# Kernel optimization log

Measured on AMD Instinct MI355X. Metric: run time of the kernel, lower is better.

## Reference

```python
import jax, jax.numpy as jnp
import numpy as np

B, L, D = 2, 2048, 2048
H, KV, HD = 16, 4, 128          # num_heads, num_kv_heads, head_dim
RD = HD // 2                    # rope_dim = 64
G = H // KV                     # GQA groups


def _rotate_half(t):
    t1, t2 = jnp.split(t, 2, axis=-1)
    return jnp.concatenate([-t2, t1], axis=-1)


def setup_inputs() -> dict:
    key = jax.random.key(0)
    ks = jax.random.split(key, 8)
    x = jax.random.normal(ks[0], (B, L, D), dtype=jnp.float32)
    # proper RoPE cos/sin tables of width RD (half-rotation layout)
    inv_freq = 1.0 / (10000.0 ** (np.arange(0, RD, 2, dtype=np.float32) / RD))
    pos = np.arange(L, dtype=np.float32)
    freqs = np.outer(pos, inv_freq)               # [L, RD/2]
    emb = np.concatenate([freqs, freqs], axis=-1)  # [L, RD]
    cos = jnp.broadcast_to(jnp.cos(emb)[None], (B, L, RD)).astype(jnp.float32)
    sin = jnp.broadcast_to(jnp.sin(emb)[None], (B, L, RD)).astype(jnp.float32)
    s = 0.02
    Wq = jax.random.normal(ks[1], (H * HD, D), dtype=jnp.float32) * s
    bq = jnp.zeros((H * HD,), dtype=jnp.float32)
    Wkv = jax.random.normal(ks[2], (KV * HD, D), dtype=jnp.float32) * s
    bkv = jnp.zeros((KV * HD,), dtype=jnp.float32)
    Wrk = jax.random.normal(ks[3], (RD, D), dtype=jnp.float32) * s
    brk = jnp.zeros((RD,), dtype=jnp.float32)
    Wo = jax.random.normal(ks[4], (D, H * HD), dtype=jnp.float32) * s
    bo = jnp.zeros((D,), dtype=jnp.float32)
    return {"x": x, "cos": cos, "sin": sin, "Wq": Wq, "bq": bq,
            "Wkv": Wkv, "bkv": bkv, "Wrk": Wrk, "brk": brk, "Wo": Wo, "bo": bo}


def reference(x, cos, sin, Wq, bq, Wkv, bkv, Wrk, brk, Wo, bo):
    Bx, Lx, _ = x.shape
    q = (x @ Wq.T + bq).reshape(Bx, Lx, H, HD)            # [B,L,H,HD]
    kv = (x @ Wkv.T + bkv).reshape(Bx, Lx, KV, HD)        # [B,L,KV,HD]
    q_nope, q_rope = q[..., : HD - RD], q[..., HD - RD:]  # [.,HD-RD],[.,RD]
    k_rope = (x @ Wrk.T + brk).reshape(Bx, Lx, 1, RD)     # [B,L,1,RD]
    c = cos[:, :, None, :]
    s = sin[:, :, None, :]
    q_rope = q_rope * c + _rotate_half(q_rope) * s
    k_rope = k_rope * c + _rotate_half(k_rope) * s
    k_rope = jnp.broadcast_to(k_rope, (Bx, Lx, KV, RD))   # tied across kv heads
    q_states = jnp.concatenate([q_nope, q_rope], axis=-1)  # [B,L,H,HD]
    kv_tied = kv[..., : HD - RD]
    k_states = jnp.concatenate([kv_tied, k_rope], axis=-1)  # [B,L,KV,HD]
    v_states = kv                                            # cat(kv_tied, tail) == kv
    # GQA causal attention, scale 1/sqrt(HD)
    qg = q_states.reshape(Bx, Lx, KV, G, HD)
    scale = 1.0 / jnp.sqrt(jnp.asarray(HD, dtype=x.dtype))
    scores = jnp.einsum('bqkgd,bskd->bkgqs', qg, k_states) * scale
    mask = jnp.tril(jnp.ones((Lx, Lx), dtype=bool))
    scores = jnp.where(mask[None, None, None], scores, jnp.finfo(scores.dtype).min)
    probs = jax.nn.softmax(scores, axis=-1)
    out = jnp.einsum('bkgqs,bskd->bqkgd', probs, v_states)
    out = out.reshape(Bx, Lx, H * HD)
    return out @ Wo.T + bo
```

## Files before the change

kernel.cpp:

```cpp
#include <hip/hip_runtime.h>
#include <hip/hip_bf16.h>

#define BB   2
#define LL   2048
#define DD   2048
#define HH   16
#define KVH  4
#define HDD  128
#define RDD  64
#define MM   (BB*LL)

typedef __attribute__((ext_vector_type(4))) float f32x4;
typedef __attribute__((ext_vector_type(8))) short bf16x8;
typedef unsigned short u16;

static __device__ __forceinline__ u16 f2b(float f) {
  __hip_bfloat16 b = __float2bfloat16(f);
  return *(const u16*)&b;
}

static __device__ __forceinline__ void gload_lds16(const void* g, void* l) {
  __builtin_amdgcn_global_load_lds(
      (const __attribute__((address_space(1))) unsigned int*)g,
      (__attribute__((address_space(3))) unsigned int*)l, 16, 0, 0);
}

#define QSCALE 0.1275174313f

__global__ __launch_bounds__(256) void cast_all(const float* __restrict__ x,
                                                const float* __restrict__ Wq,
                                                const float* __restrict__ Wkv,
                                                const float* __restrict__ Wrk,
                                                const float* __restrict__ Wo,
                                                u16* __restrict__ xb, u16* __restrict__ Wqb,
                                                u16* __restrict__ Wkvb, u16* __restrict__ Wrkb,
                                                u16* __restrict__ Wob) {
  const int i = blockIdx.x * 256 + threadIdx.x;
  const float* src; u16* dst; int off;
  if (i < 2097152)      { src = x;   dst = xb;   off = i; }
  else if (i < 3145728) { src = Wq;  dst = Wqb;  off = i - 2097152; }
  else if (i < 3407872) { src = Wkv; dst = Wkvb; off = i - 3145728; }
  else if (i < 3440640) { src = Wrk; dst = Wrkb; off = i - 3407872; }
  else                  { src = Wo;  dst = Wob;  off = i - 3440640; }
  float4 v = ((const float4*)src)[off];
  ushort4 o;
  o.x = f2b(v.x); o.y = f2b(v.y); o.z = f2b(v.z); o.w = f2b(v.w);
  ((ushort4*)dst)[off] = o;
}

__global__ __launch_bounds__(256) void gemm128(const u16* __restrict__ A,
                                               const u16* __restrict__ W,
                                               const float* __restrict__ bias,
                                               float* __restrict__ C,
                                               int M, int N, int K) {
  __shared__ u16 As[128 * 32];
  __shared__ u16 Bs[128 * 32];
  const int w = threadIdx.x >> 6, lane = threadIdx.x & 63;
  const int r = lane & 15, hi = lane >> 4, rg = hi * 4;
  const int wm = w >> 1, wn = w & 1;
  const int m0 = blockIdx.y * 128, n0 = blockIdx.x * 128;
  const int srow = w * 32 + (lane >> 2);
  const int scb  = (lane & 3) * 16;
  f32x4 acc[4][4];
#pragma unroll
  for (int i = 0; i < 4; ++i)
#pragma unroll
    for (int j = 0; j < 4; ++j) acc[i][j] = (f32x4){0.f, 0.f, 0.f, 0.f};

  for (int k0 = 0; k0 < K; k0 += 32) {
#pragma unroll
    for (int i = 0; i < 2; ++i) {
      gload_lds16((const char*)(A + (size_t)(m0 + srow + i * 16) * K + k0) + scb,
                  (char*)As + (w * 2 + i) * 1024);
      gload_lds16((const char*)(W + (size_t)(n0 + srow + i * 16) * K + k0) + scb,
                  (char*)Bs + (w * 2 + i) * 1024);
    }
    __syncthreads();
    bf16x8 a[4], b[4];
#pragma unroll
    for (int i = 0; i < 4; ++i)
      a[i] = *(const bf16x8*)((const char*)As + (wm * 64 + i * 16 + r) * 64 + hi * 16);
#pragma unroll
    for (int j = 0; j < 4; ++j)
      b[j] = *(const bf16x8*)((const char*)Bs + (wn * 64 + j * 16 + r) * 64 + hi * 16);
#pragma unroll
    for (int i = 0; i < 4; ++i)
#pragma unroll
      for (int j = 0; j < 4; ++j)
        acc[i][j] = __builtin_amdgcn_mfma_f32_16x16x32_bf16(a[i], b[j], acc[i][j], 0, 0, 0);
    __syncthreads();
  }
#pragma unroll
  for (int j = 0; j < 4; ++j) {
    const float bv = bias[n0 + wn * 64 + j * 16 + r];
#pragma unroll
    for (int i = 0; i < 4; ++i)
#pragma unroll
      for (int ii = 0; ii < 4; ++ii)
        C[(size_t)(m0 + wm * 64 + i * 16 + rg + ii) * N + n0 + wn * 64 + j * 16 + r] =
            acc[i][j][ii] + bv;
  }
}

__global__ __launch_bounds__(256) void gemm_q_fused(const u16* __restrict__ A,
                                                    const u16* __restrict__ W,
                                                    const float* __restrict__ bias,
                                                    const float* __restrict__ cosb,
                                                    const float* __restrict__ sinb,
                                                    u16* __restrict__ Qb) {
  __shared__ u16 As[128 * 32];
  __shared__ u16 Bs[128 * 32];
  const int w = threadIdx.x >> 6, lane = threadIdx.x & 63;
  const int r = lane & 15, hi = lane >> 4, rg = hi * 4;
  const int wm = w >> 1, wn = w & 1;
  const int h = blockIdx.x;
  const int m0 = blockIdx.y * 128, n0 = h * 128;
  const int srow = w * 32 + (lane >> 2);
  const int scb  = (lane & 3) * 16;
  f32x4 acc[4][4];
#pragma unroll
  for (int i = 0; i < 4; ++i)
#pragma unroll
    for (int j = 0; j < 4; ++j) acc[i][j] = (f32x4){0.f, 0.f, 0.f, 0.f};

  for (int k0 = 0; k0 < DD; k0 += 32) {
#pragma unroll
    for (int i = 0; i < 2; ++i) {
      gload_lds16((const char*)(A + (size_t)(m0 + srow + i * 16) * DD + k0) + scb,
                  (char*)As + (w * 2 + i) * 1024);
      gload_lds16((const char*)(W + (size_t)(n0 + srow + i * 16) * DD + k0) + scb,
                  (char*)Bs + (w * 2 + i) * 1024);
    }
    __syncthreads();
    bf16x8 a[4], b[4];
#pragma unroll
    for (int i = 0; i < 4; ++i)
      a[i] = *(const bf16x8*)((const char*)As + (wm * 64 + i * 16 + r) * 64 + hi * 16);
#pragma unroll
    for (int j = 0; j < 4; ++j)
      b[j] = *(const bf16x8*)((const char*)Bs + (wn * 64 + j * 16 + r) * 64 + hi * 16);
#pragma unroll
    for (int i = 0; i < 4; ++i)
#pragma unroll
      for (int j = 0; j < 4; ++j)
        acc[i][j] = __builtin_amdgcn_mfma_f32_16x16x32_bf16(a[i], b[j], acc[i][j], 0, 0, 0);
    __syncthreads();
  }

  const int b = m0 >> 11;
  const int lbase = (m0 & 2047) + wm * 64;
  u16* Qimg = Qb + (size_t)((b * 16 + h) * 128) * 2048;
  if (wn == 0) {
#pragma unroll
    for (int j = 0; j < 4; ++j) {
      const int d = j * 16 + r;
      const float bv = bias[h * 128 + d];
#pragma unroll
      for (int i = 0; i < 4; ++i)
#pragma unroll
        for (int ii = 0; ii < 4; ++ii) {
          const int l = lbase + i * 16 + rg + ii;
          Qimg[(size_t)(l >> 4) * 2048 + (d >> 5) * 512 + ((d >> 3) & 3) * 128 +
               (l & 15) * 8 + (d & 7)] = f2b((acc[i][j][ii] + bv) * QSCALE);
        }
    }
  } else {
#pragma unroll
    for (int jp = 0; jp < 2; ++jp) {
      const int dd0 = jp * 16 + r;
      const int dd1 = dd0 + 32;
      const float bv0 = bias[h * 128 + 64 + dd0];
      const float bv1 = bias[h * 128 + 64 + dd1];
#pragma unroll
      for (int i = 0; i < 4; ++i)
#pragma unroll
        for (int ii = 0; ii < 4; ++ii) {
          const int l = lbase + i * 16 + rg + ii;
          const size_t nb = (size_t)(b * 2048 + l) * 64;
          const float c0 = cosb[nb + dd0], s0 = sinb[nb + dd0];
          const float c1 = cosb[nb + dd1], s1 = sinb[nb + dd1];
          const float a0 = acc[i][jp][ii] + bv0;
          const float a1 = acc[i][jp + 2][ii] + bv1;
          const float v0 = (a0 * c0 - a1 * s0) * QSCALE;
          const float v1 = (a1 * c1 + a0 * s1) * QSCALE;
          const int d0f = 64 + dd0, d1f = 64 + dd1;
          const size_t rowoff = (size_t)(l >> 4) * 2048 + (l & 15) * 8;
          Qimg[rowoff + (d0f >> 5) * 512 + ((d0f >> 3) & 3) * 128 + (d0f & 7)] = f2b(v0);
          Qimg[rowoff + (d1f >> 5) * 512 + ((d1f >> 3) & 3) * 128 + (d1f & 7)] = f2b(v1);
        }
    }
  }
}

__global__ __launch_bounds__(256) void gemm_kv_fused(const u16* __restrict__ A,
                                                     const u16* __restrict__ W,
                                                     const float* __restrict__ bias,
                                                     u16* __restrict__ Kb,
                                                     u16* __restrict__ VTb) {
  __shared__ u16 As[128 * 32];
  __shared__ u16 Bs[128 * 32];
  const int w = threadIdx.x >> 6, lane = threadIdx.x & 63;
  const int r = lane & 15, hi = lane >> 4, rg = hi * 4;
  const int wm = w >> 1, wn = w & 1;
  const int c = blockIdx.x;
  const int m0 = blockIdx.y * 128, n0 = c * 128;
  const int srow = w * 32 + (lane >> 2);
  const int scb  = (lane & 3) * 16;
  f32x4 acc[4][4];
#pragma unroll
  for (int i = 0; i < 4; ++i)
#pragma unroll
    for (int j = 0; j < 4; ++j) acc[i][j] = (f32x4){0.f, 0.f, 0.f, 0.f};

  for (int k0 = 0; k0 < DD; k0 += 32) {
#pragma unroll
    for (int i = 0; i < 2; ++i) {
      gload_lds16((const char*)(A + (size_t)(m0 + srow + i * 16) * DD + k0) + scb,
                  (char*)As + (w * 2 + i) * 1024);
      gload_lds16((const char*)(W + (size_t)(n0 + srow + i * 16) * DD + k0) + scb,
                  (char*)Bs + (w * 2 + i) * 1024);
    }
    __syncthreads();
    bf16x8 a[4], b[4];
#pragma unroll
    for (int i = 0; i < 4; ++i)
      a[i] = *(const bf16x8*)((const char*)As + (wm * 64 + i * 16 + r) * 64 + hi * 16);
#pragma unroll
    for (int j = 0; j < 4; ++j)
      b[j] = *(const bf16x8*)((const char*)Bs + (wn * 64 + j * 16 + r) * 64 + hi * 16);
#pragma unroll
    for (int i = 0; i < 4; ++i)
#pragma unroll
      for (int j = 0; j < 4; ++j)
        acc[i][j] = __builtin_amdgcn_mfma_f32_16x16x32_bf16(a[i], b[j], acc[i][j], 0, 0, 0);
    __syncthreads();
  }

  const int b = m0 >> 11;
  const int lbase = (m0 & 2047) + wm * 64;
  u16* Kimg = Kb + (size_t)(b * KVH + c) * 32 * 8192;
  u16* Vimg = VTb + (size_t)(b * KVH + c) * 32 * 8192;
#pragma unroll
  for (int j = 0; j < 4; ++j) {
    const int d = wn * 64 + j * 16 + r;
    const float bv = bias[c * 128 + d];
#pragma unroll
    for (int i = 0; i < 4; ++i)
#pragma unroll
      for (int ii = 0; ii < 4; ++ii) {
        const int l = lbase + i * 16 + rg + ii;
        const u16 bf = f2b(acc[i][j][ii] + bv);
        const int lt = l & 63;
        Vimg[(size_t)(l >> 6) * 8192 + ((d >> 4) * 2 + ((lt >> 5) & 1)) * 512 +
             ((lt >> 2) & 3) * 128 + (d & 15) * 8 + ((lt >> 4) & 1) * 4 + (lt & 3)] = bf;
        if (wn == 0)
          Kimg[(size_t)(l >> 6) * 8192 + ((lt >> 4) & 3) * 2048 + (d >> 5) * 512 +
               ((d >> 3) & 3) * 128 + (lt & 15) * 8 + (d & 7)] = bf;
      }
  }
}

__global__ __launch_bounds__(256) void gemm_rk_fused(const u16* __restrict__ A,
                                                     const u16* __restrict__ Wrkb,
                                                     const float* __restrict__ brk,
                                                     const float* __restrict__ cosb,
                                                     const float* __restrict__ sinb,
                                                     u16* __restrict__ Kb) {
  __shared__ f32x4 red[4][2][64];
  const int w = threadIdx.x >> 6, lane = threadIdx.x & 63;
  const int bx = blockIdx.x;
  const int m0 = blockIdx.y * 16;
  const int r = lane & 15;
  const int kq = (lane >> 4) * 8;
  const u16* ap  = A + (size_t)(m0 + r) * DD + kq;
  const u16* wp0 = Wrkb + (size_t)(bx * 16 + r) * DD + kq;
  const u16* wp1 = Wrkb + (size_t)(bx * 16 + 32 + r) * DD + kq;
  f32x4 acc0 = {0.f, 0.f, 0.f, 0.f}, acc1 = {0.f, 0.f, 0.f, 0.f};
  for (int k = w * 512; k < w * 512 + 512; k += 32) {
    bf16x8 a  = *(const bf16x8*)(ap + k);
    bf16x8 b0 = *(const bf16x8*)(wp0 + k);
    bf16x8 b1 = *(const bf16x8*)(wp1 + k);
    acc0 = __builtin_amdgcn_mfma_f32_16x16x32_bf16(a, b0, acc0, 0, 0, 0);
    acc1 = __builtin_amdgcn_mfma_f32_16x16x32_bf16(a, b1, acc1, 0, 0, 0);
  }
  red[w][0][lane] = acc0;
  red[w][1][lane] = acc1;
  __syncthreads();
  if (w == 0) {
#pragma unroll
    for (int ww = 1; ww < 4; ++ww) {
      acc0 += red[ww][0][lane];
      acc1 += red[ww][1][lane];
    }
    const int rg = (lane >> 4) * 4;
    const int dd0 = bx * 16 + r, dd1 = dd0 + 32;
    const float bv0 = brk[dd0], bv1 = brk[dd1];
    const int d0f = 64 + dd0, d1f = 64 + dd1;
#pragma unroll
    for (int i = 0; i < 4; ++i) {
      const int n = m0 + rg + i;
      const int b = n >> 11, l = n & 2047;
      const size_t nb = (size_t)n * 64;
      const float c0 = cosb[nb + dd0], s0 = sinb[nb + dd0];
      const float c1 = cosb[nb + dd1], s1 = sinb[nb + dd1];
      const float a0 = acc0[i] + bv0;
      const float a1 = acc1[i] + bv1;
      const u16 v0 = f2b(a0 * c0 - a1 * s0);
      const u16 v1 = f2b(a1 * c1 + a0 * s1);
      const int lt = l & 63;
      const size_t loff = (size_t)(l >> 6) * 8192 + ((lt >> 4) & 3) * 2048 + (lt & 15) * 8;
#pragma unroll
      for (int c = 0; c < 4; ++c) {
        u16* Kimg = Kb + (size_t)(b * KVH + c) * 32 * 8192;
        Kimg[loff + (d0f >> 5) * 512 + ((d0f >> 3) & 3) * 128 + (d0f & 7)] = v0;
        Kimg[loff + (d1f >> 5) * 512 + ((d1f >> 3) & 3) * 128 + (d1f & 7)] = v1;
      }
    }
  }
}

static __device__ __forceinline__ void stage_g(const u16* Kt, const u16* Vt,
                                               char* GB, int buf, int wg, int lane) {
#pragma unroll
  for (int i = 0; i < 4; ++i) {
    const int j = wg * 4 + i;
    gload_lds16(Kt + (size_t)j * 512 + lane * 8, (u16*)(GB + buf * 16384) + j * 512);
    gload_lds16(Vt + (size_t)j * 512 + lane * 8, (u16*)(GB + 32768 + buf * 16384) + j * 512);
  }
}

__global__ __launch_bounds__(512, 2) void attn_mfma10(const u16* __restrict__ Qb,
                                                      const u16* __restrict__ Kb,
                                                      const u16* __restrict__ VTb,
                                                      u16* __restrict__ attn_bf) {
  const int id = blockIdx.x;
  const int g = id & 31;
  const int s = id >> 5;
  const int bc = g & 7, hlow = g >> 3;
  const int b = bc >> 2, c = bc & 3;
  const int h = c * 4 + hlow;
  const int bh = b * 16 + h;
  const int w = threadIdx.x >> 6, lane = threadIdx.x & 63;
  const int r = lane & 15, hi = lane >> 4, rg = hi * 4;
  const int grp = w >> 2, wg = w & 3;

  __shared__ __align__(16) char LB[131072];
  char* GB = LB + grp * 65536;

  const u16* Ktg = Kb + (size_t)(b * KVH + c) * 32 * 8192;
  const u16* Vtg = VTb + (size_t)(b * KVH + c) * 32 * 8192;

  for (int ss = 0; ss < 2; ++ss) {
    const int qb = ss ? s : (15 - s);
    const int q0 = qb * 128 + wg * 32;
    const int half = qb + 1;
    const int tb = grp ? half : 0;

    bf16x8 qf[2][4];
#pragma unroll
    for (int qs = 0; qs < 2; ++qs) {
      const u16* qtb = Qb + (size_t)(bh * 128 + qb * 8 + wg * 2 + qs) * 2048;
#pragma unroll
      for (int ks = 0; ks < 4; ++ks)
        qf[qs][ks] = *(const bf16x8*)(qtb + ks * 512 + lane * 8);
    }

    float m_[2] = {-3.0e38f, -3.0e38f}, l_[2] = {0.f, 0.f};
    f32x4 o[2][8];
#pragma unroll
    for (int qs = 0; qs < 2; ++qs)
#pragma unroll
      for (int t = 0; t < 8; ++t) o[qs][t] = (f32x4){0.f, 0.f, 0.f, 0.f};

    stage_g(Ktg + (size_t)tb * 8192, Vtg + (size_t)tb * 8192, GB, 0, wg, lane);
    __syncthreads();
    int cur = 0;

    for (int t = 0; t < half; ++t) {
      if (t + 1 < half)
        stage_g(Ktg + (size_t)(tb + t + 1) * 8192, Vtg + (size_t)(tb + t + 1) * 8192,
                GB, cur ^ 1, wg, lane);
      const int s0 = (tb + t) * 64;

      if (s0 <= q0 + 31) {
        const u16* Kl = (const u16*)(GB + cur * 16384);
        const u16* Vl = (const u16*)(GB + 32768 + cur * 16384);

        f32x4 st[2][4];
#pragma unroll
        for (int qs = 0; qs < 2; ++qs)
#pragma unroll
          for (int tt = 0; tt < 4; ++tt) st[qs][tt] = (f32x4){0.f, 0.f, 0.f, 0.f};
        __builtin_amdgcn_s_setprio(1);
#pragma unroll
        for (int tt = 0; tt < 4; ++tt) {
          bf16x8 kf[4];
#pragma unroll
          for (int ks = 0; ks < 4; ++ks)
            kf[ks] = *(const bf16x8*)(Kl + tt * 2048 + ks * 512 + lane * 8);
#pragma unroll
          for (int qs = 0; qs < 2; ++qs)
#pragma unroll
            for (int ks = 0; ks < 4; ++ks)
              st[qs][tt] = __builtin_amdgcn_mfma_f32_16x16x32_bf16(kf[ks], qf[qs][ks], st[qs][tt], 0, 0, 0);
        }
        __builtin_amdgcn_s_setprio(0);

        if (s0 + 63 > q0) {
#pragma unroll
          for (int qs = 0; qs < 2; ++qs)
#pragma unroll
            for (int tt = 0; tt < 4; ++tt)
#pragma unroll
              for (int i = 0; i < 4; ++i)
                if (s0 + tt * 16 + rg + i > q0 + qs * 16 + r) st[qs][tt][i] = -3.0e38f;
        }

        float vmax[2];
#pragma unroll
        for (int qs = 0; qs < 2; ++qs) {
          float v = st[qs][0][0];
#pragma unroll
          for (int tt = 0; tt < 4; ++tt)
#pragma unroll
            for (int i = 0; i < 4; ++i) v = fmaxf(v, st[qs][tt][i]);
          v = fmaxf(v, __shfl_xor(v, 16));
          v = fmaxf(v, __shfl_xor(v, 32));
          vmax[qs] = v;
        }
        const float grow = fmaxf(vmax[0] - m_[0], vmax[1] - m_[1]);
        if (!__all(grow <= 11.54f)) {
#pragma unroll
          for (int qs = 0; qs < 2; ++qs) {
            const float mn = fmaxf(m_[qs], vmax[qs]);
            const float cf = exp2f(m_[qs] - mn);
            l_[qs] *= cf;
            m_[qs] = mn;
#pragma unroll
            for (int tt = 0; tt < 8; ++tt)
#pragma unroll
              for (int i = 0; i < 4; ++i) o[qs][tt][i] *= cf;
          }
        }
        bf16x8 pa[2][2];
#pragma unroll
        for (int qs = 0; qs < 2; ++qs) {
          float ps = 0.f;
#pragma unroll
          for (int tt = 0; tt < 4; ++tt)
#pragma unroll
            for (int i = 0; i < 4; ++i) {
              st[qs][tt][i] = exp2f(st[qs][tt][i] - m_[qs]);
              ps += st[qs][tt][i];
            }
          ps += __shfl_xor(ps, 16);
          ps += __shfl_xor(ps, 32);
          l_[qs] += ps;
#pragma unroll
          for (int kb = 0; kb < 2; ++kb) {
            bf16x8 v;
#pragma unroll
            for (int jj = 0; jj < 8; ++jj)
              v[jj] = (short)f2b(st[qs][2 * kb + (jj >> 2)][jj & 3]);
            pa[qs][kb] = v;
          }
        }

        __builtin_amdgcn_s_setprio(1);
#pragma unroll
        for (int tt = 0; tt < 8; ++tt) {
#pragma unroll
          for (int kb = 0; kb < 2; ++kb) {
            bf16x8 vf = *(const bf16x8*)(Vl + tt * 1024 + kb * 512 + lane * 8);
#pragma unroll
            for (int qs = 0; qs < 2; ++qs)
              o[qs][tt] = __builtin_amdgcn_mfma_f32_16x16x32_bf16(pa[qs][kb], vf, o[qs][tt], 0, 0, 0);
          }
        }
        __builtin_amdgcn_s_setprio(0);
      }

      __syncthreads();
      cur ^= 1;
    }

    float2* mlp = (float2*)(LB + 65536);
    if (hi == 0) {
      mlp[(w * 2 + 0) * 16 + r] = make_float2(m_[0], l_[0]);
      mlp[(w * 2 + 1) * 16 + r] = make_float2(m_[1], l_[1]);
    }
    __syncthreads();
    float lC[2], asc[2];
#pragma unroll
    for (int qs = 0; qs < 2; ++qs) {
      const float2 p = mlp[((w ^ 4) * 2 + qs) * 16 + r];
      const float mn = fmaxf(m_[qs], p.x);
      const float a1 = exp2f(m_[qs] - mn);
      lC[qs] = l_[qs] * a1 + p.y * exp2f(p.x - mn);
      asc[qs] = a1;
    }
#pragma unroll
    for (int qs = 0; qs < 2; ++qs) {
      float ai[4];
#pragma unroll
      for (int i = 0; i < 4; ++i) ai[i] = __shfl(asc[qs], (lane & 48) + rg + i);
#pragma unroll
      for (int tt = 0; tt < 8; ++tt)
#pragma unroll
        for (int i = 0; i < 4; ++i) o[qs][tt][i] *= ai[i];
    }
    if (grp == 1) {
#pragma unroll
      for (int qs = 0; qs < 2; ++qs)
#pragma unroll
        for (int tt = 0; tt < 8; ++tt)
          *(f32x4*)(LB + wg * 16384 + (qs * 8 + tt) * 1024 + lane * 16) = o[qs][tt];
    }
    __syncthreads();
    if (grp == 0) {
#pragma unroll
      for (int qs = 0; qs < 2; ++qs) {
#pragma unroll
        for (int tt = 0; tt < 8; ++tt)
          o[qs][tt] += *(const f32x4*)(LB + wg * 16384 + (qs * 8 + tt) * 1024 + lane * 16);
        const float il = 1.f / lC[qs];
        float inv[4];
#pragma unroll
        for (int i = 0; i < 4; ++i) inv[i] = __shfl(il, (lane & 48) + rg + i);
        u16* op = attn_bf + (size_t)(b * LL + q0 + qs * 16 + rg) * DD + h * HDD;
#pragma unroll
        for (int tt = 0; tt < 8; ++tt)
#pragma unroll
          for (int i = 0; i < 4; ++i)
            op[(size_t)i * DD + tt * 16 + r] = f2b(o[qs][tt][i] * inv[i]);
      }
    }
    __syncthreads();
  }
}

extern "C" void kernel_launch(void* const* d_in, const int* in_sizes, int n_in,
                              void* d_out, int out_size, void* d_ws, size_t ws_size,
                              hipStream_t stream) {
  const float* x    = (const float*)d_in[0];
  const float* cosb = (const float*)d_in[1];
  const float* sinb = (const float*)d_in[2];
  const float* Wq   = (const float*)d_in[3];
  const float* bq   = (const float*)d_in[4];
  const float* Wkv  = (const float*)d_in[5];
  const float* bkv  = (const float*)d_in[6];
  const float* Wrk  = (const float*)d_in[7];
  const float* brk  = (const float*)d_in[8];
  const float* Wo   = (const float*)d_in[9];
  const float* bo   = (const float*)d_in[10];
  float* out = (float*)d_out;

  char* ws = (char*)d_ws;
  u16*   Qb    = (u16*)(ws);
  u16*   attn_bf = (u16*)(ws + 16777216);
  u16*   xb    = (u16*)(ws + 33554432);
  u16*   Wqb   = (u16*)(ws + 50331648);
  u16*   Wob   = (u16*)(ws + 58720256);
  u16*   Wkvb  = (u16*)(ws + 67108864);
  u16*   Wrkb  = (u16*)(ws + 69206016);
  u16*   Kb    = (u16*)(ws + 70516736);
  u16*   VTb   = (u16*)(ws + 74711040);

  cast_all<<<17536, 256, 0, stream>>>(x, Wq, Wkv, Wrk, Wo, xb, Wqb, Wkvb, Wrkb, Wob);

  gemm_q_fused<<<dim3(HH, MM / 128), 256, 0, stream>>>(xb, Wqb, bq, cosb, sinb, Qb);
  gemm_kv_fused<<<dim3(KVH, MM / 128), 256, 0, stream>>>(xb, Wkvb, bkv, Kb, VTb);
  gemm_rk_fused<<<dim3(2, MM / 16), 256, 0, stream>>>(xb, Wrkb, brk, cosb, sinb, Kb);

  attn_mfma10<<<dim3(256), 512, 0, stream>>>(Qb, Kb, VTb, attn_bf);

  gemm128<<<dim3(DD / 128, MM / 128), 256, 0, stream>>>(attn_bf, Wob, bo, out, MM, DD, DD);
}
```

Baseline: 231.5 us.

## Split attention KV range across four wave groups with 32-row KV tiles

The attention kernel now runs 1024 threads per block, with four wave groups each covering a quarter of the causal KV range, instead of two groups covering halves. KV tiles shrink from 64 to 32 rows, so the K/V image layouts written by the projection GEMMs change to match. The final softmax merge combines four partial (m,l) pairs and reduces outputs through LDS in two stages. This is meant to shorten the per-block serial KV loop and add waves for latency hiding, at the cost of one block per CU, smaller MFMA batches per sync, and a longer merge.

Result: slower. 363.1 us (+56.9%).

```diff
diff --git a/kernel.cpp b/kernel.cpp
--- a/kernel.cpp
+++ b/kernel.cpp
@@ -238,8 +238,8 @@
 
   const int b = m0 >> 11;
   const int lbase = (m0 & 2047) + wm * 64;
-  u16* Kimg = Kb + (size_t)(b * KVH + c) * 32 * 8192;
-  u16* Vimg = VTb + (size_t)(b * KVH + c) * 32 * 8192;
+  u16* Kimg = Kb + (size_t)(b * KVH + c) * 64 * 4096;
+  u16* Vimg = VTb + (size_t)(b * KVH + c) * 64 * 4096;
 #pragma unroll
   for (int j = 0; j < 4; ++j) {
     const int d = wn * 64 + j * 16 + r;
@@ -250,11 +250,11 @@
       for (int ii = 0; ii < 4; ++ii) {
         const int l = lbase + i * 16 + rg + ii;
         const u16 bf = f2b(acc[i][j][ii] + bv);
-        const int lt = l & 63;
-        Vimg[(size_t)(l >> 6) * 8192 + ((d >> 4) * 2 + ((lt >> 5) & 1)) * 512 +
-             ((lt >> 2) & 3) * 128 + (d & 15) * 8 + ((lt >> 4) & 1) * 4 + (lt & 3)] = bf;
+        const int lt = l & 31;
+        Vimg[(size_t)(l >> 5) * 4096 + (d >> 4) * 512 + ((lt >> 2) & 3) * 128 +
+             (d & 15) * 8 + ((lt >> 4) & 1) * 4 + (lt & 3)] = bf;
         if (wn == 0)
-          Kimg[(size_t)(l >> 6) * 8192 + ((lt >> 4) & 3) * 2048 + (d >> 5) * 512 +
+          Kimg[(size_t)(l >> 5) * 4096 + ((lt >> 4) & 1) * 2048 + (d >> 5) * 512 +
                ((d >> 3) & 3) * 128 + (lt & 15) * 8 + (d & 7)] = bf;
       }
   }
@@ -307,11 +307,11 @@
       const float a1 = acc1[i] + bv1;
       const u16 v0 = f2b(a0 * c0 - a1 * s0);
       const u16 v1 = f2b(a1 * c1 + a0 * s1);
-      const int lt = l & 63;
-      const size_t loff = (size_t)(l >> 6) * 8192 + ((lt >> 4) & 3) * 2048 + (lt & 15) * 8;
+      const int lt = l & 31;
+      const size_t loff = (size_t)(l >> 5) * 4096 + ((lt >> 4) & 1) * 2048 + (lt & 15) * 8;
 #pragma unroll
       for (int c = 0; c < 4; ++c) {
-        u16* Kimg = Kb + (size_t)(b * KVH + c) * 32 * 8192;
+        u16* Kimg = Kb + (size_t)(b * KVH + c) * 64 * 4096;
         Kimg[loff + (d0f >> 5) * 512 + ((d0f >> 3) & 3) * 128 + (d0f & 7)] = v0;
         Kimg[loff + (d1f >> 5) * 512 + ((d1f >> 3) & 3) * 128 + (d1f & 7)] = v1;
       }
@@ -322,17 +322,17 @@
 static __device__ __forceinline__ void stage_g(const u16* Kt, const u16* Vt,
                                                char* GB, int buf, int wg, int lane) {
 #pragma unroll
-  for (int i = 0; i < 4; ++i) {
-    const int j = wg * 4 + i;
-    gload_lds16(Kt + (size_t)j * 512 + lane * 8, (u16*)(GB + buf * 16384) + j * 512);
-    gload_lds16(Vt + (size_t)j * 512 + lane * 8, (u16*)(GB + 32768 + buf * 16384) + j * 512);
-  }
-}
-
-__global__ __launch_bounds__(512, 2) void attn_mfma10(const u16* __restrict__ Qb,
-                                                      const u16* __restrict__ Kb,
-                                                      const u16* __restrict__ VTb,
-                                                      u16* __restrict__ attn_bf) {
+  for (int i = 0; i < 2; ++i) {
+    const int j = wg * 2 + i;
+    gload_lds16(Kt + (size_t)j * 512 + lane * 8, (u16*)(GB + buf * 8192) + j * 512);
+    gload_lds16(Vt + (size_t)j * 512 + lane * 8, (u16*)(GB + 16384 + buf * 8192) + j * 512);
+  }
+}
+
+__global__ __launch_bounds__(1024, 1) void attn_mfma12(const u16* __restrict__ Qb,
+                                                       const u16* __restrict__ Kb,
+                                                       const u16* __restrict__ VTb,
+                                                       u16* __restrict__ attn_bf) {
   const int id = blockIdx.x;
   const int g = id & 31;
   const int s = id >> 5;
@@ -344,17 +344,17 @@
   const int r = lane & 15, hi = lane >> 4, rg = hi * 4;
   const int grp = w >> 2, wg = w & 3;
 
-  __shared__ __align__(16) char LB[131072];
-  char* GB = LB + grp * 65536;
-
-  const u16* Ktg = Kb + (size_t)(b * KVH + c) * 32 * 8192;
-  const u16* Vtg = VTb + (size_t)(b * KVH + c) * 32 * 8192;
+  __shared__ __align__(16) char LB[135168];
+  char* GB = LB + grp * 32768;
+
+  const u16* Ktg = Kb + (size_t)(b * KVH + c) * 64 * 4096;
+  const u16* Vtg = VTb + (size_t)(b * KVH + c) * 64 * 4096;
 
   for (int ss = 0; ss < 2; ++ss) {
     const int qb = ss ? s : (15 - s);
     const int q0 = qb * 128 + wg * 32;
     const int half = qb + 1;
-    const int tb = grp ? half : 0;
+    const int tb = grp * half;
 
     bf16x8 qf[2][4];
 #pragma unroll
@@ -372,28 +372,28 @@
 #pragma unroll
       for (int t = 0; t < 8; ++t) o[qs][t] = (f32x4){0.f, 0.f, 0.f, 0.f};
 
-    stage_g(Ktg + (size_t)tb * 8192, Vtg + (size_t)tb * 8192, GB, 0, wg, lane);
+    stage_g(Ktg + (size_t)tb * 4096, Vtg + (size_t)tb * 4096, GB, 0, wg, lane);
     __syncthreads();
     int cur = 0;
 
     for (int t = 0; t < half; ++t) {
       if (t + 1 < half)
-        stage_g(Ktg + (size_t)(tb + t + 1) * 8192, Vtg + (size_t)(tb + t + 1) * 8192,
+        stage_g(Ktg + (size_t)(tb + t + 1) * 4096, Vtg + (size_t)(tb + t + 1) * 4096,
                 GB, cur ^ 1, wg, lane);
-      const int s0 = (tb + t) * 64;
+      const int s0 = (tb + t) * 32;
 
       if (s0 <= q0 + 31) {
-        const u16* Kl = (const u16*)(GB + cur * 16384);
-        const u16* Vl = (const u16*)(GB + 32768 + cur * 16384);
-
-        f32x4 st[2][4];
+        const u16* Kl = (const u16*)(GB + cur * 8192);
+        const u16* Vl = (const u16*)(GB + 16384 + cur * 8192);
+
+        f32x4 st[2][2];
 #pragma unroll
         for (int qs = 0; qs < 2; ++qs)
 #pragma unroll
-          for (int tt = 0; tt < 4; ++tt) st[qs][tt] = (f32x4){0.f, 0.f, 0.f, 0.f};
+          for (int tt = 0; tt < 2; ++tt) st[qs][tt] = (f32x4){0.f, 0.f, 0.f, 0.f};
         __builtin_amdgcn_s_setprio(1);
 #pragma unroll
-        for (int tt = 0; tt < 4; ++tt) {
+        for (int tt = 0; tt < 2; ++tt) {
           bf16x8 kf[4];
 #pragma unroll
           for (int ks = 0; ks < 4; ++ks)
@@ -406,11 +406,11 @@
         }
         __builtin_amdgcn_s_setprio(0);
 
-        if (s0 + 63 > q0) {
+        if (s0 + 31 > q0) {
 #pragma unroll
           for (int qs = 0; qs < 2; ++qs)
 #pragma unroll
-            for (int tt = 0; tt < 4; ++tt)
+            for (int tt = 0; tt < 2; ++tt)
 #pragma unroll
               for (int i = 0; i < 4; ++i)
                 if (s0 + tt * 16 + rg + i > q0 + qs * 16 + r) st[qs][tt][i] = -3.0e38f;
@@ -421,7 +421,7 @@
         for (int qs = 0; qs < 2; ++qs) {
           float v = st[qs][0][0];
 #pragma unroll
-          for (int tt = 0; tt < 4; ++tt)
+          for (int tt = 0; tt < 2; ++tt)
 #pragma unroll
             for (int i = 0; i < 4; ++i) v = fmaxf(v, st[qs][tt][i]);
           v = fmaxf(v, __shfl_xor(v, 16));
@@ -442,12 +442,12 @@
               for (int i = 0; i < 4; ++i) o[qs][tt][i] *= cf;
           }
         }
-        bf16x8 pa[2][2];
+        bf16x8 pa[2];
 #pragma unroll
         for (int qs = 0; qs < 2; ++qs) {
           float ps = 0.f;
 #pragma unroll
-          for (int tt = 0; tt < 4; ++tt)
+          for (int tt = 0; tt < 2; ++tt)
 #pragma unroll
             for (int i = 0; i < 4; ++i) {
               st[qs][tt][i] = exp2f(st[qs][tt][i] - m_[qs]);
@@ -456,26 +456,20 @@
           ps += __shfl_xor(ps, 16);
           ps += __shfl_xor(ps, 32);
           l_[qs] += ps;
-#pragma unroll
-          for (int kb = 0; kb < 2; ++kb) {
-            bf16x8 v;
-#pragma unroll
-            for (int jj = 0; jj < 8; ++jj)
-              v[jj] = (short)f2b(st[qs][2 * kb + (jj >> 2)][jj & 3]);
-            pa[qs][kb] = v;
-          }
+          bf16x8 v;
+#pragma unroll
+          for (int jj = 0; jj < 8; ++jj)
+            v[jj] = (short)f2b(st[qs][jj >> 2][jj & 3]);
+          pa[qs] = v;
         }
 
         __builtin_amdgcn_s_setprio(1);
 #pragma unroll
-        for (int tt = 0; tt < 8; ++tt) {
-#pragma unroll
-          for (int kb = 0; kb < 2; ++kb) {
-            bf16x8 vf = *(const bf16x8*)(Vl + tt * 1024 + kb * 512 + lane * 8);
-#pragma unroll
-            for (int qs = 0; qs < 2; ++qs)
-              o[qs][tt] = __builtin_amdgcn_mfma_f32_16x16x32_bf16(pa[qs][kb], vf, o[qs][tt], 0, 0, 0);
-          }
+        for (int dt = 0; dt < 8; ++dt) {
+          bf16x8 vf = *(const bf16x8*)(Vl + dt * 512 + lane * 8);
+#pragma unroll
+          for (int qs = 0; qs < 2; ++qs)
+            o[qs][dt] = __builtin_amdgcn_mfma_f32_16x16x32_bf16(pa[qs], vf, o[qs][dt], 0, 0, 0);
         }
         __builtin_amdgcn_s_setprio(0);
       }
@@ -484,45 +478,70 @@
       cur ^= 1;
     }
 
-    float2* mlp = (float2*)(LB + 65536);
+    float2* mlp = (float2*)(LB + 131072);
     if (hi == 0) {
       mlp[(w * 2 + 0) * 16 + r] = make_float2(m_[0], l_[0]);
       mlp[(w * 2 + 1) * 16 + r] = make_float2(m_[1], l_[1]);
     }
     __syncthreads();
-    float lC[2], asc[2];
+    float lC[2], aown[2];
 #pragma unroll
     for (int qs = 0; qs < 2; ++qs) {
-      const float2 p = mlp[((w ^ 4) * 2 + qs) * 16 + r];
-      const float mn = fmaxf(m_[qs], p.x);
-      const float a1 = exp2f(m_[qs] - mn);
-      lC[qs] = l_[qs] * a1 + p.y * exp2f(p.x - mn);
-      asc[qs] = a1;
+      float mn = -3.0e38f;
+      float2 e[4];
+#pragma unroll
+      for (int gg = 0; gg < 4; ++gg) {
+        e[gg] = mlp[((gg * 4 + wg) * 2 + qs) * 16 + r];
+        mn = fmaxf(mn, e[gg].x);
+      }
+      float ls = 0.f;
+#pragma unroll
+      for (int gg = 0; gg < 4; ++gg) ls += e[gg].y * exp2f(e[gg].x - mn);
+      lC[qs] = ls;
+      aown[qs] = exp2f(m_[qs] - mn);
     }
 #pragma unroll
     for (int qs = 0; qs < 2; ++qs) {
       float ai[4];
 #pragma unroll
-      for (int i = 0; i < 4; ++i) ai[i] = __shfl(asc[qs], (lane & 48) + rg + i);
+      for (int i = 0; i < 4; ++i) ai[i] = __shfl(aown[qs], (lane & 48) + rg + i);
 #pragma unroll
       for (int tt = 0; tt < 8; ++tt)
 #pragma unroll
         for (int i = 0; i < 4; ++i) o[qs][tt][i] *= ai[i];
     }
-    if (grp == 1) {
+    if (grp == 1 || grp == 3) {
+      char* dstR = LB + (grp == 1 ? 0 : 65536);
 #pragma unroll
       for (int qs = 0; qs < 2; ++qs)
 #pragma unroll
         for (int tt = 0; tt < 8; ++tt)
-          *(f32x4*)(LB + wg * 16384 + (qs * 8 + tt) * 1024 + lane * 16) = o[qs][tt];
+          *(f32x4*)(dstR + wg * 16384 + (qs * 8 + tt) * 1024 + lane * 16) = o[qs][tt];
     }
     __syncthreads();
     if (grp == 0) {
 #pragma unroll
-      for (int qs = 0; qs < 2; ++qs) {
+      for (int qs = 0; qs < 2; ++qs)
 #pragma unroll
         for (int tt = 0; tt < 8; ++tt)
           o[qs][tt] += *(const f32x4*)(LB + wg * 16384 + (qs * 8 + tt) * 1024 + lane * 16);
+    } else if (grp == 2) {
+#pragma unroll
+      for (int qs = 0; qs < 2; ++qs)
+#pragma unroll
+        for (int tt = 0; tt < 8; ++tt) {
+          f32x4* p = (f32x4*)(LB + 65536 + wg * 16384 + (qs * 8 + tt) * 1024 + lane * 16);
+          o[qs][tt] += *p;
+          *p = o[qs][tt];
+        }
+    }
+    __syncthreads();
+    if (grp == 0) {
+#pragma unroll
+      for (int qs = 0; qs < 2; ++qs) {
+#pragma unroll
+        for (int tt = 0; tt < 8; ++tt)
+          o[qs][tt] += *(const f32x4*)(LB + 65536 + wg * 16384 + (qs * 8 + tt) * 1024 + lane * 16);
         const float il = 1.f / lC[qs];
         float inv[4];
 #pragma unroll
@@ -572,7 +591,7 @@
   gemm_kv_fused<<<dim3(KVH, MM / 128), 256, 0, stream>>>(xb, Wkvb, bkv, Kb, VTb);
   gemm_rk_fused<<<dim3(2, MM / 16), 256, 0, stream>>>(xb, Wrkb, brk, cosb, sinb, Kb);
 
-  attn_mfma10<<<dim3(256), 512, 0, stream>>>(Qb, Kb, VTb, attn_bf);
+  attn_mfma12<<<dim3(256), 1024, 0, stream>>>(Qb, Kb, VTb, attn_bf);
 
   gemm128<<<dim3(DD / 128, MM / 128), 256, 0, stream>>>(attn_bf, Wob, bo, out, MM, DD, DD);
 }
```
